# Kernel tuning notes

Hardware: AMD Instinct MI355X
Metric: run time of the kernel (lower is better)

Reference implementation:

```python
import jax, jax.numpy as jnp
import numpy as np

D = 1024
H = 16
HD = D // H  # 64


def gelu_custom(x):
    # Note: module uses 0.04715 (not the standard 0.044715) -- replicate exactly.
    c = jnp.sqrt(jnp.asarray(2.0 / jnp.pi, dtype=x.dtype))
    return 0.5 * x * (1.0 + jnp.tanh(c * (x + 0.04715 * x ** 3)))


def layernorm(x, scale, shift, eps=1e-5):
    u = jnp.mean(x, axis=-1, keepdims=True)
    v = jnp.var(x, axis=-1, keepdims=True)
    return scale * ((x - u) / jnp.sqrt(v + eps)) + shift


def setup_inputs() -> dict:
    key = jax.random.key(0)
    ks = jax.random.split(key, 12)
    s = 0.02
    X = jax.random.normal(ks[0], (4, 2048, D), dtype=jnp.float32)
    Wq = jax.random.normal(ks[1], (D, D), dtype=jnp.float32) * s
    Wk = jax.random.normal(ks[2], (D, D), dtype=jnp.float32) * s
    Wv = jax.random.normal(ks[3], (D, D), dtype=jnp.float32) * s
    Wo = jax.random.normal(ks[4], (D, D), dtype=jnp.float32) * s
    bo = jnp.zeros((D,), dtype=jnp.float32)
    W1 = jax.random.normal(ks[5], (D, 4 * D), dtype=jnp.float32) * s
    b1 = jnp.zeros((4 * D,), dtype=jnp.float32)
    W2 = jax.random.normal(ks[6], (4 * D, D), dtype=jnp.float32) * s
    b2 = jnp.zeros((D,), dtype=jnp.float32)
    g1 = jnp.ones((D,), dtype=jnp.float32)
    s1 = jnp.zeros((D,), dtype=jnp.float32)
    g2 = jnp.ones((D,), dtype=jnp.float32)
    s2 = jnp.zeros((D,), dtype=jnp.float32)
    return {"X": X, "Wq": Wq, "Wk": Wk, "Wv": Wv, "Wo": Wo, "bo": bo,
            "W1": W1, "b1": b1, "W2": W2, "b2": b2,
            "g1": g1, "s1": s1, "g2": g2, "s2": s2}


def reference(X, Wq, Wk, Wv, Wo, bo, W1, b1, W2, b2, g1, s1, g2, s2):
    b, n, _ = X.shape
    # --- pre-LN attention sublayer ---
    shortcut = X
    Y = layernorm(X, g1, s1)
    Q = (Y @ Wq).reshape(b, n, H, HD).transpose(0, 2, 1, 3)  # [b,h,n,hd]
    K = (Y @ Wk).reshape(b, n, H, HD).transpose(0, 2, 1, 3)
    V = (Y @ Wv).reshape(b, n, H, HD).transpose(0, 2, 1, 3)
    S = jnp.einsum('bhqd,bhkd->bhqk', Q, K)  # full eager score matrix
    causal = jnp.triu(jnp.ones((n, n), dtype=bool), k=1)
    S = jnp.where(causal, -jnp.inf, S)
    W = jax.nn.softmax(S / jnp.sqrt(jnp.asarray(HD, dtype=S.dtype)), axis=-1)
    Z = jnp.einsum('bhqk,bhkd->bhqd', W, V)
    Z = Z.transpose(0, 2, 1, 3).reshape(b, n, D)
    Z = Z @ Wo + bo
    X1 = Z + shortcut
    # --- pre-LN FFN sublayer ---
    Y2 = layernorm(X1, g2, s2)
    F = gelu_custom(Y2 @ W1 + b1) @ W2 + b2
    return F + X1
```

## Files before the change

### kernel.cpp

```cpp
#include <hip/hip_runtime.h>
#include <cstdint>
#include <cstddef>

#define DEV static __device__ __forceinline__

typedef __bf16 bf16x8 __attribute__((ext_vector_type(8)));
typedef float f32x4 __attribute__((ext_vector_type(4)));
typedef unsigned short u16x8 __attribute__((ext_vector_type(8)));
typedef unsigned short u16;

DEV u16 f2bf(float f) { __bf16 b = (__bf16)f; return __builtin_bit_cast(u16, b); }

DEV void async_cp16(const void* g, void* l) {
    __builtin_amdgcn_global_load_lds(
        (const __attribute__((address_space(1))) void*)g,
        (__attribute__((address_space(3))) void*)l, 16, 0, 0);
}

DEV void wait_vm6() { asm volatile("s_waitcnt vmcnt(6)" ::: "memory"); }
DEV void wait_vm4() { asm volatile("s_waitcnt vmcnt(4)" ::: "memory"); }
DEV void wait_vm0() { asm volatile("s_waitcnt vmcnt(0)" ::: "memory"); }

DEV float gelu_fn(float x) {
    const float c = 0.7978845608028654f;
    float t = c * (x + 0.04715f * x * x * x);
    float e = __expf(2.f * t);
    float th = 1.f - 2.f / (e + 1.f);
    return 0.5f * x * (1.f + th);
}

__global__ __launch_bounds__(256) void wtrans_all_kernel(
    const float* __restrict__ Wq, const float* __restrict__ Wk,
    const float* __restrict__ Wv, const float* __restrict__ Wo,
    const float* __restrict__ W1, const float* __restrict__ W2,
    u16* __restrict__ Wqkvt, u16* __restrict__ Wot,
    u16* __restrict__ W1t, u16* __restrict__ W2t)
{
    const int bid = blockIdx.x;
    const float* W;
    u16* Wt;
    int K, N, nx, loc;
    if (bid < 4096) {
        loc = bid & 1023;
        const int wsel = bid >> 10;
        W = (wsel == 0) ? Wq : (wsel == 1) ? Wk : (wsel == 2) ? Wv : Wo;
        Wt = (wsel == 3) ? Wot : (Wqkvt + (size_t)wsel * 1024 * 1024);
        K = 1024; N = 1024; nx = 32;
    } else if (bid < 8192) {
        loc = bid - 4096; W = W1; Wt = W1t; K = 1024; N = 4096; nx = 128;
    } else {
        loc = bid - 8192; W = W2; Wt = W2t; K = 4096; N = 1024; nx = 32;
    }
    const int n0 = (loc % nx) * 32, k0 = (loc / nx) * 32;

    __shared__ float t[32][33];
    const int tx = threadIdx.x & 31, ty = threadIdx.x >> 5;
#pragma unroll
    for (int i = 0; i < 4; ++i)
        t[ty + i * 8][tx] = W[(size_t)(k0 + ty + i * 8) * N + n0 + tx];
    __syncthreads();
#pragma unroll
    for (int i = 0; i < 4; ++i)
        Wt[(size_t)(n0 + ty + i * 8) * K + k0 + tx] = f2bf(t[tx][ty + i * 8]);
}

__global__ __launch_bounds__(256) void ln_kernel(
    const float* __restrict__ X, const float* __restrict__ g,
    const float* __restrict__ sh, u16* __restrict__ Y)
{
    int row = blockIdx.x;
    const float4* xr = (const float4*)(X + (size_t)row * 1024);
    float4 x = xr[threadIdx.x];
    float s = x.x + x.y + x.z + x.w;
    float ss = x.x * x.x + x.y * x.y + x.z * x.z + x.w * x.w;
#pragma unroll
    for (int off = 32; off >= 1; off >>= 1) {
        s += __shfl_xor(s, off);
        ss += __shfl_xor(ss, off);
    }
    __shared__ float ps[4], pss[4];
    int wave = threadIdx.x >> 6, lane = threadIdx.x & 63;
    if (lane == 0) { ps[wave] = s; pss[wave] = ss; }
    __syncthreads();
    s = ps[0] + ps[1] + ps[2] + ps[3];
    ss = pss[0] + pss[1] + pss[2] + pss[3];
    float mean = s * (1.f / 1024.f);
    float var = ss * (1.f / 1024.f) - mean * mean;
    float rstd = rsqrtf(var + 1e-5f);
    int c = threadIdx.x * 4;
    ushort4 o;
    o.x = f2bf((x.x - mean) * rstd * g[c + 0] + sh[c + 0]);
    o.y = f2bf((x.y - mean) * rstd * g[c + 1] + sh[c + 1]);
    o.z = f2bf((x.z - mean) * rstd * g[c + 2] + sh[c + 2]);
    o.w = f2bf((x.w - mean) * rstd * g[c + 3] + sh[c + 3]);
    ((ushort4*)(Y + (size_t)row * 1024))[threadIdx.x] = o;
}

template <int OUT_BF16, int HAS_BIAS, int HAS_RES, int ACT_GELU>
__global__ __launch_bounds__(256) void gemm_kernel(
    const u16* __restrict__ A, const u16* __restrict__ Bt,
    const float* __restrict__ bias, const float* __restrict__ res,
    void* __restrict__ Cout, int M, int N, int K)
{
    __shared__ u16 As[3][128 * 32];
    __shared__ u16 Bs[3][128 * 32];
    const int tid = threadIdx.x;
    const int lane = tid & 63, wave = tid >> 6;
    const int wm = wave >> 1, wn = wave & 1;
    const int l16 = lane & 15, lg = lane >> 4;
    const int rowBase = blockIdx.y * 128;
    const int colBase = blockIdx.x * 128;

    f32x4 acc[4][4];
#pragma unroll
    for (int m = 0; m < 4; ++m)
#pragma unroll
        for (int n = 0; n < 4; ++n) acc[m][n] = (f32x4){0.f, 0.f, 0.f, 0.f};

#define GSTAGE(SB, KT)                                                        \
    {                                                                         \
        _Pragma("unroll")                                                     \
        for (int i_ = 0; i_ < 2; ++i_) {                                      \
            int eo = tid * 8 + i_ * 2048;                                     \
            int r_ = eo >> 5, c_ = eo & 31;                                   \
            async_cp16(A + (size_t)(rowBase + r_) * K + (KT) + c_, As[SB] + eo); \
            async_cp16(Bt + (size_t)(colBase + r_) * K + (KT) + c_, Bs[SB] + eo); \
        }                                                                     \
    }

    const int nt = K >> 5;
    GSTAGE(0, 0);
    GSTAGE(1, 32);
    wait_vm4();
    __builtin_amdgcn_s_barrier();
    __builtin_amdgcn_sched_barrier(0);

    int cur = 0, stg = 2;
    for (int t = 0; t < nt; ++t) {
        const bool more = (t + 2 < nt);
        if (more) GSTAGE(stg, (t + 2) * 32);

        bf16x8 af[4], bfr[4];
#pragma unroll
        for (int m = 0; m < 4; ++m)
            af[m] = *(const bf16x8*)(As[cur] + (wm * 64 + m * 16 + l16) * 32 + lg * 8);
#pragma unroll
        for (int n = 0; n < 4; ++n)
            bfr[n] = *(const bf16x8*)(Bs[cur] + (wn * 64 + n * 16 + l16) * 32 + lg * 8);
#pragma unroll
        for (int m = 0; m < 4; ++m)
#pragma unroll
            for (int n = 0; n < 4; ++n)
                acc[m][n] = __builtin_amdgcn_mfma_f32_16x16x32_bf16(
                    af[m], bfr[n], acc[m][n], 0, 0, 0);

        if (more) wait_vm4(); else wait_vm0();
        __builtin_amdgcn_s_barrier();
        __builtin_amdgcn_sched_barrier(0);
        cur = (cur == 2) ? 0 : cur + 1;
        stg = (stg == 2) ? 0 : stg + 1;
    }
#undef GSTAGE

#pragma unroll
    for (int m = 0; m < 4; ++m) {
#pragma unroll
        for (int n = 0; n < 4; ++n) {
            int gr0 = rowBase + wm * 64 + m * 16 + lg * 4;
            int gc = colBase + wn * 64 + n * 16 + l16;
            float bv = HAS_BIAS ? bias[gc] : 0.f;
#pragma unroll
            for (int r = 0; r < 4; ++r) {
                float v = acc[m][n][r] + bv;
                if (ACT_GELU) v = gelu_fn(v);
                if (HAS_RES) v += res[(size_t)(gr0 + r) * N + gc];
                if (OUT_BF16)
                    ((u16*)Cout)[(size_t)(gr0 + r) * N + gc] = f2bf(v);
                else
                    ((float*)Cout)[(size_t)(gr0 + r) * N + gc] = v;
            }
        }
    }
}

template <int OUT_BF16, int HAS_BIAS, int ACT_GELU>
__global__ __launch_bounds__(512, 2) void gemm8p_kernel(
    const u16* __restrict__ A, const u16* __restrict__ Bt,
    const float* __restrict__ bias, void* __restrict__ Cout,
    int M, int N, int K)
{
    __shared__ u16 As[2][256 * 64];
    __shared__ u16 Bs[2][256 * 64];
    const int tid = threadIdx.x;
    const int lane = tid & 63, wave = tid >> 6;
    const int wm = wave >> 2, wn = wave & 3;
    const int l16 = lane & 15, lg = lane >> 4;

    const int gx = gridDim.x, gy = gridDim.y;
    const int nwg = gx * gy;
    const int orig = (int)blockIdx.y * gx + (int)blockIdx.x;
    const int work = (orig & 7) * (nwg >> 3) + (orig >> 3);
    const int colBase = (work / gy) * 256;
    const int rowBase = (work % gy) * 256;

    f32x4 acc[8][4];
#pragma unroll
    for (int m = 0; m < 8; ++m)
#pragma unroll
        for (int n = 0; n < 4; ++n) acc[m][n] = (f32x4){0.f, 0.f, 0.f, 0.f};

#define STRIP(SB, KT, S)                                                      \
    {                                                                         \
        int tl_ = tid & 255, hf_ = tid >> 8;                                  \
        int r_ = hf_ * 128 + (S) * 32 + (tl_ >> 3);                           \
        int gl_ = (tl_ & 7) ^ (r_ & 7);                                       \
        int dst_ = r_ * 64 + (tl_ & 7) * 8;                                   \
        async_cp16(A + (size_t)(rowBase + r_) * K + (KT) + gl_ * 8, As[SB] + dst_); \
        async_cp16(Bt + (size_t)(colBase + r_) * K + (KT) + gl_ * 8, Bs[SB] + dst_); \
    }
#define FRAG_OFF(row, G) ((row) * 64 + (((G) ^ ((row) & 7)) * 8))

#define PHASE(BUF, QUAD, LOADB, STAGE, WAITN)                                 \
    {                                                                         \
        __builtin_amdgcn_sched_barrier(0);                                    \
        if (LOADB) {                                                          \
            _Pragma("unroll")                                                 \
            for (int nf = 0; nf < 4; ++nf) {                                  \
                int row = wn * 64 + nf * 16 + l16;                            \
                _Pragma("unroll")                                             \
                for (int ks = 0; ks < 2; ++ks)                                \
                    bfr[nf][ks] = *(const bf16x8*)(Bs[BUF] + FRAG_OFF(row, lg + ks * 4)); \
            }                                                                 \
        }                                                                     \
        bf16x8 af[2][2];                                                      \
        _Pragma("unroll")                                                     \
        for (int mi = 0; mi < 2; ++mi) {                                      \
            int row = wm * 128 + (QUAD) * 32 + mi * 16 + l16;                 \
            _Pragma("unroll")                                                 \
            for (int ks = 0; ks < 2; ++ks)                                    \
                af[mi][ks] = *(const bf16x8*)(As[BUF] + FRAG_OFF(row, lg + ks * 4)); \
        }                                                                     \
        STAGE;                                                                \
        __builtin_amdgcn_sched_barrier(0);                                    \
        __builtin_amdgcn_s_barrier();                                         \
        __builtin_amdgcn_s_setprio(1);                                        \
        _Pragma("unroll")                                                     \
        for (int mi = 0; mi < 2; ++mi)                                        \
            _Pragma("unroll")                                                 \
            for (int nf = 0; nf < 4; ++nf)                                    \
                _Pragma("unroll")                                             \
                for (int ks = 0; ks < 2; ++ks)                                \
                    acc[(QUAD) * 2 + mi][nf] =                                \
                        __builtin_amdgcn_mfma_f32_16x16x32_bf16(              \
                            af[mi][ks], bfr[nf][ks], acc[(QUAD) * 2 + mi][nf], 0, 0, 0); \
        __builtin_amdgcn_s_setprio(0);                                        \
        __builtin_amdgcn_sched_barrier(0);                                    \
        WAITN;                                                                \
        __builtin_amdgcn_s_barrier();                                         \
    }

    const int nt = K >> 6;
    const int half = nt >> 1;

    STRIP(0, 0, 0); STRIP(0, 0, 1); STRIP(0, 0, 2); STRIP(0, 0, 3);
    STRIP(1, 64, 0); STRIP(1, 64, 1); STRIP(1, 64, 2);
    wait_vm6();
    __builtin_amdgcn_s_barrier();
    __builtin_amdgcn_sched_barrier(0);

    for (int it = 0; it < half; ++it) {
        const int kt1 = (it * 2 + 1) << 6;
        const int kt2 = (it * 2 + 2) << 6;
        const int kt3 = (it * 2 + 3) << 6;
        const bool more = (it + 1 < half);
        bf16x8 bfr[4][2];
        PHASE(0, 0, 1, STRIP(1, kt1, 3), ((void)0));
        PHASE(0, 1, 0, if (more) STRIP(0, kt2, 0), ((void)0));
        PHASE(0, 2, 0, if (more) STRIP(0, kt2, 1), ((void)0));
        PHASE(0, 3, 0, if (more) STRIP(0, kt2, 2),
              if (more) wait_vm6(); else wait_vm0());
        PHASE(1, 0, 1, if (more) STRIP(0, kt2, 3), ((void)0));
        PHASE(1, 1, 0, if (more) STRIP(1, kt3, 0), ((void)0));
        PHASE(1, 2, 0, if (more) STRIP(1, kt3, 1), ((void)0));
        PHASE(1, 3, 0, if (more) STRIP(1, kt3, 2),
              if (more) wait_vm6(); else wait_vm0());
    }
#undef STRIP
#undef FRAG_OFF
#undef PHASE

#pragma unroll
    for (int mf = 0; mf < 8; ++mf) {
#pragma unroll
        for (int nf = 0; nf < 4; ++nf) {
            int gr0 = rowBase + wm * 128 + mf * 16 + lg * 4;
            int gc = colBase + wn * 64 + nf * 16 + l16;
            float bv = HAS_BIAS ? bias[gc] : 0.f;
#pragma unroll
            for (int r = 0; r < 4; ++r) {
                float v = acc[mf][nf][r] + bv;
                if (ACT_GELU) v = gelu_fn(v);
                if (OUT_BF16)
                    ((u16*)Cout)[(size_t)(gr0 + r) * N + gc] = f2bf(v);
                else
                    ((float*)Cout)[(size_t)(gr0 + r) * N + gc] = v;
            }
        }
    }
}

__global__ __launch_bounds__(512) void attn_kernel(
    const u16* __restrict__ QKV, u16* __restrict__ Z)
{
    __shared__ u16 Ks[2][64 * 64];
    __shared__ u16 Vt[2][64 * 64];
    __shared__ u16 Pl[8][32 * 64];

    const int bh = blockIdx.x;
    const int b = bh >> 4, h = bh & 15;
    const int g = blockIdx.y;
    const int qt = (g < 4) ? (7 - g) : (g - 4);
    const int tid = threadIdx.x;
    const int wave = tid >> 6, lane = tid & 63;
    const int l16 = lane & 15, lg = lane >> 4;

    const size_t baseQ = (size_t)b * 2048 * 3072 + (size_t)h * 64;
    const size_t baseK = baseQ + 1024;
    const size_t baseV = baseQ + 2048;

    const int q0w = qt * 256 + wave * 32;

    bf16x8 aq[2][2];
#pragma unroll
    for (int mq = 0; mq < 2; ++mq) {
        const u16* qp = QKV + baseQ + (size_t)(q0w + mq * 16 + l16) * 3072;
#pragma unroll
        for (int hf = 0; hf < 2; ++hf) {
            bf16x8 v = *(const bf16x8*)(qp + hf * 32 + lg * 8);
#pragma unroll
            for (int j = 0; j < 8; ++j) v[j] = (__bf16)((float)v[j] * 0.125f);
            aq[mq][hf] = v;
        }
    }

    f32x4 o[2][4];
    float lrow[2][4];
#pragma unroll
    for (int mq = 0; mq < 2; ++mq)
#pragma unroll
        for (int i = 0; i < 4; ++i) {
            o[mq][i] = (f32x4){0.f, 0.f, 0.f, 0.f};
            lrow[mq][i] = 0.f;
        }

    const int nch = 4 * qt + 4;

#define STAGE_K(BUF, KB)                                                      \
    {                                                                         \
        int n = tid;                                                          \
        int r = n >> 3;                                                       \
        int lb = ((n & 7) * 16) ^ ((r & 7) << 4);                             \
        async_cp16(QKV + baseK + (size_t)((KB) + r) * 3072 + (lb >> 1),       \
                   Ks[BUF] + n * 8);                                          \
    }
#define LOAD_V(KB, V0)                                                        \
    {                                                                         \
        const u16* vp = QKV + baseV + (size_t)((KB) + lane) * 3072;           \
        V0 = *(const u16x8*)(vp + wave * 8);                                  \
    }
#define WRITE_V(BUF, V0)                                                      \
    {                                                                         \
        _Pragma("unroll")                                                     \
        for (int j = 0; j < 8; ++j) {                                         \
            int d = wave * 8 + j;                                             \
            int byt = (d * 128 + lane * 2) ^ ((d & 7) << 4);                  \
            Vt[BUF][byt >> 1] = V0[j];                                        \
        }                                                                     \
    }
#define SOFTMAX_BODY(DIAG)                                                    \
    _Pragma("unroll")                                                         \
    for (int mq = 0; mq < 2; ++mq) {                                          \
        _Pragma("unroll")                                                     \
        for (int r = 0; r < 4; ++r) {                                         \
            float sv0 = s[mq][0][r];                                          \
            float sv1 = s[mq][1][r];                                          \
            float sv2 = s[mq][2][r];                                          \
            float sv3 = s[mq][3][r];                                          \
            if (DIAG) {                                                       \
                const int q = q0w + mq * 16 + lg * 4 + r;                     \
                if (kbase + 0 + l16 > q)  sv0 = -1e30f;                       \
                if (kbase + 16 + l16 > q) sv1 = -1e30f;                       \
                if (kbase + 32 + l16 > q) sv2 = -1e30f;                       \
                if (kbase + 48 + l16 > q) sv3 = -1e30f;                       \
            }                                                                 \
            float p0 = __expf(sv0), p1 = __expf(sv1);                         \
            float p2 = __expf(sv2), p3 = __expf(sv3);                         \
            lrow[mq][r] += (p0 + p1) + (p2 + p3);                             \
            int rowm = mq * 16 + lg * 4 + r;                                  \
            int rb = rowm * 128, swz = (rowm & 7) << 4;                       \
            Pl[wave][(rb + ((0  + 2 * l16) ^ swz)) >> 1] = f2bf(p0);          \
            Pl[wave][(rb + ((32 + 2 * l16) ^ swz)) >> 1] = f2bf(p1);          \
            Pl[wave][(rb + ((64 + 2 * l16) ^ swz)) >> 1] = f2bf(p2);          \
            Pl[wave][(rb + ((96 + 2 * l16) ^ swz)) >> 1] = f2bf(p3);          \
        }                                                                     \
    }

    {
        STAGE_K(0, 0);
        u16x8 v0;
        LOAD_V(0, v0);
        WRITE_V(0, v0);
    }
    __syncthreads();

    int cur = 0;
    for (int kc = 0; kc < nch; ++kc) {
        const int kbase = kc * 64;
        const int nxt = cur ^ 1;
        const bool more = (kc + 1 < nch);
        u16x8 nv0;
        if (more) {
            STAGE_K(nxt, kbase + 64);
            LOAD_V(kbase + 64, nv0);
        }

        if (q0w + 31 >= kbase) {
            f32x4 s[2][4];
#pragma unroll
            for (int mq = 0; mq < 2; ++mq)
#pragma unroll
                for (int t = 0; t < 4; ++t) s[mq][t] = (f32x4){0.f, 0.f, 0.f, 0.f};
            __builtin_amdgcn_s_setprio(1);
#pragma unroll
            for (int t = 0; t < 4; ++t) {
                int row = t * 16 + l16;
                int swz = (row & 7) << 4;
                bf16x8 bk0 = *(const bf16x8*)(Ks[cur] + ((row * 128 + ((16 * lg) ^ swz)) >> 1));
                bf16x8 bk1 = *(const bf16x8*)(Ks[cur] + ((row * 128 + ((64 + 16 * lg) ^ swz)) >> 1));
#pragma unroll
                for (int mq = 0; mq < 2; ++mq) {
                    s[mq][t] = __builtin_amdgcn_mfma_f32_16x16x32_bf16(aq[mq][0], bk0, s[mq][t], 0, 0, 0);
                    s[mq][t] = __builtin_amdgcn_mfma_f32_16x16x32_bf16(aq[mq][1], bk1, s[mq][t], 0, 0, 0);
                }
            }
            __builtin_amdgcn_s_setprio(0);

            const bool diag = (kbase + 63 > q0w);
            if (diag) { SOFTMAX_BODY(1) } else { SOFTMAX_BODY(0) }

            bf16x8 bv[2][4];
#pragma unroll
            for (int kst = 0; kst < 2; ++kst)
#pragma unroll
                for (int ct = 0; ct < 4; ++ct) {
                    int d = ct * 16 + l16;
                    bv[kst][ct] = *(const bf16x8*)(Vt[cur] + ((d * 128 + ((64 * kst + 16 * lg) ^ ((d & 7) << 4))) >> 1));
                }
            __builtin_amdgcn_s_setprio(1);
#pragma unroll
            for (int mq = 0; mq < 2; ++mq) {
                int rowm = mq * 16 + l16;
                int swz = (rowm & 7) << 4;
                bf16x8 ap0 = *(const bf16x8*)(&Pl[wave][(rowm * 128 + ((16 * lg) ^ swz)) >> 1]);
                bf16x8 ap1 = *(const bf16x8*)(&Pl[wave][(rowm * 128 + ((64 + 16 * lg) ^ swz)) >> 1]);
#pragma unroll
                for (int ct = 0; ct < 4; ++ct) {
                    o[mq][ct] = __builtin_amdgcn_mfma_f32_16x16x32_bf16(ap0, bv[0][ct], o[mq][ct], 0, 0, 0);
                    o[mq][ct] = __builtin_amdgcn_mfma_f32_16x16x32_bf16(ap1, bv[1][ct], o[mq][ct], 0, 0, 0);
                }
            }
            __builtin_amdgcn_s_setprio(0);
        }

        if (more) { WRITE_V(nxt, nv0); }
        __syncthreads();
        cur = nxt;
    }

#pragma unroll
    for (int mq = 0; mq < 2; ++mq)
#pragma unroll
        for (int r = 0; r < 4; ++r) {
            float l = lrow[mq][r];
            l += __shfl_xor(l, 1);
            l += __shfl_xor(l, 2);
            l += __shfl_xor(l, 4);
            l += __shfl_xor(l, 8);
            float inv = 1.f / l;
            size_t zr = ((size_t)b * 2048 + q0w + mq * 16 + lg * 4 + r) * 1024 + h * 64;
#pragma unroll
            for (int ct = 0; ct < 4; ++ct)
                Z[zr + ct * 16 + l16] = f2bf(o[mq][ct][r] * inv);
        }
#undef STAGE_K
#undef LOAD_V
#undef WRITE_V
#undef SOFTMAX_BODY
}

extern "C" void kernel_launch(void* const* d_in, const int* in_sizes, int n_in,
                              void* d_out, int out_size, void* d_ws, size_t ws_size,
                              hipStream_t stream)
{
    const float* X  = (const float*)d_in[0];
    const float* Wq = (const float*)d_in[1];
    const float* Wk = (const float*)d_in[2];
    const float* Wv = (const float*)d_in[3];
    const float* Wo = (const float*)d_in[4];
    const float* bo = (const float*)d_in[5];
    const float* W1 = (const float*)d_in[6];
    const float* b1 = (const float*)d_in[7];
    const float* W2 = (const float*)d_in[8];
    const float* b2 = (const float*)d_in[9];
    const float* g1 = (const float*)d_in[10];
    const float* s1 = (const float*)d_in[11];
    const float* g2 = (const float*)d_in[12];
    const float* s2 = (const float*)d_in[13];
    float* out = (float*)d_out;

    uint8_t* ws = (uint8_t*)d_ws;
    const size_t MB = 1024 * 1024;
    u16* Wqkvt = (u16*)(ws + 0 * MB);
    u16* Wot   = (u16*)(ws + 6 * MB);
    u16* W1t   = (u16*)(ws + 8 * MB);
    u16* W2t   = (u16*)(ws + 16 * MB);
    u16* Yb    = (u16*)(ws + 24 * MB);
    u16* QKVb  = (u16*)(ws + 40 * MB);
    u16* Zb    = (u16*)(ws + 24 * MB);
    u16* Y2b   = (u16*)(ws + 40 * MB);
    u16* Hb    = (u16*)(ws + 56 * MB);

    wtrans_all_kernel<<<12288, 256, 0, stream>>>(Wq, Wk, Wv, Wo, W1, W2,
                                                 Wqkvt, Wot, W1t, W2t);

    ln_kernel<<<8192, 256, 0, stream>>>(X, g1, s1, Yb);

    gemm_kernel<1, 0, 0, 0><<<dim3(24, 64), 256, 0, stream>>>(Yb, Wqkvt, nullptr, nullptr, QKVb, 8192, 3072, 1024);

    attn_kernel<<<dim3(64, 8), 512, 0, stream>>>(QKVb, Zb);

    gemm_kernel<0, 1, 1, 0><<<dim3(8, 64), 256, 0, stream>>>(Zb, Wot, bo, X, out, 8192, 1024, 1024);

    ln_kernel<<<8192, 256, 0, stream>>>(out, g2, s2, Y2b);

    gemm8p_kernel<1, 1, 1><<<dim3(16, 32), 512, 0, stream>>>(Y2b, W1t, b1, Hb, 8192, 4096, 1024);

    gemm_kernel<0, 1, 1, 0><<<dim3(8, 64), 256, 0, stream>>>(Hb, W2t, b2, out, out, 8192, 1024, 4096);
}
```

Baseline: 408.4 us.

## Run FFN down-projection with split-K on the 256x256 GEMM plus combine kernel

The W2 GEMM (K=4096) moves from the 128x128 gemm_kernel to the larger 256x256 gemm8p kernel with a 2-way split-K. Each half writes a bf16 partial into the workspace, and a new combine kernel adds both partials, the bias and the residual into the output. The goal is to use the more efficient large-tile kernel while still launching enough workgroups (256) to fill the device. In exchange it adds an extra kernel launch and extra memory traffic for the partials. Storing the partials in bf16 also loses some precision before accumulation.

New measurement: 381.1 us. -6.7%, faster.

```diff
diff --git a/kernel.cpp b/kernel.cpp
--- a/kernel.cpp
+++ b/kernel.cpp
@@ -10,6 +10,7 @@
 typedef unsigned short u16;
 
 DEV u16 f2bf(float f) { __bf16 b = (__bf16)f; return __builtin_bit_cast(u16, b); }
+DEV float bf2f(u16 u) { unsigned v = (unsigned)u << 16; return __builtin_bit_cast(float, v); }
 
 DEV void async_cp16(const void* g, void* l) {
     __builtin_amdgcn_global_load_lds(
@@ -96,6 +97,23 @@
     ((ushort4*)(Y + (size_t)row * 1024))[threadIdx.x] = o;
 }
 
+__global__ __launch_bounds__(256) void combine_kernel(
+    const u16* __restrict__ P0, const u16* __restrict__ P1,
+    const float* __restrict__ b2, float* __restrict__ out)
+{
+    const size_t row = blockIdx.x;
+    const int c = threadIdx.x * 4;
+    const size_t off = row * 1024 + c;
+    ushort4 a = *(const ushort4*)(P0 + off);
+    ushort4 b = *(const ushort4*)(P1 + off);
+    float4 o = *(float4*)(out + off);
+    o.x += bf2f(a.x) + bf2f(b.x) + b2[c + 0];
+    o.y += bf2f(a.y) + bf2f(b.y) + b2[c + 1];
+    o.z += bf2f(a.z) + bf2f(b.z) + b2[c + 2];
+    o.w += bf2f(a.w) + bf2f(b.w) + b2[c + 3];
+    *(float4*)(out + off) = o;
+}
+
 template <int OUT_BF16, int HAS_BIAS, int HAS_RES, int ACT_GELU>
 __global__ __launch_bounds__(256) void gemm_kernel(
     const u16* __restrict__ A, const u16* __restrict__ Bt,
@@ -187,7 +205,7 @@
 __global__ __launch_bounds__(512, 2) void gemm8p_kernel(
     const u16* __restrict__ A, const u16* __restrict__ Bt,
     const float* __restrict__ bias, void* __restrict__ Cout,
-    int M, int N, int K)
+    int M, int N, int K, int ldk, int rowTiles, int koff, size_t coff)
 {
     __shared__ u16 As[2][256 * 64];
     __shared__ u16 Bs[2][256 * 64];
@@ -201,7 +219,11 @@
     const int orig = (int)blockIdx.y * gx + (int)blockIdx.x;
     const int work = (orig & 7) * (nwg >> 3) + (orig >> 3);
     const int colBase = (work / gy) * 256;
-    const int rowBase = (work % gy) * 256;
+    const int wy = work % gy;
+    const int rowBase = (wy % rowTiles) * 256;
+    const int ks = wy / rowTiles;
+    A += (size_t)ks * koff;
+    Bt += (size_t)ks * koff;
 
     f32x4 acc[8][4];
 #pragma unroll
@@ -215,8 +237,8 @@
         int r_ = hf_ * 128 + (S) * 32 + (tl_ >> 3);                           \
         int gl_ = (tl_ & 7) ^ (r_ & 7);                                       \
         int dst_ = r_ * 64 + (tl_ & 7) * 8;                                   \
-        async_cp16(A + (size_t)(rowBase + r_) * K + (KT) + gl_ * 8, As[SB] + dst_); \
-        async_cp16(Bt + (size_t)(colBase + r_) * K + (KT) + gl_ * 8, Bs[SB] + dst_); \
+        async_cp16(A + (size_t)(rowBase + r_) * ldk + (KT) + gl_ * 8, As[SB] + dst_); \
+        async_cp16(Bt + (size_t)(colBase + r_) * ldk + (KT) + gl_ * 8, Bs[SB] + dst_); \
     }
 #define FRAG_OFF(row, G) ((row) * 64 + (((G) ^ ((row) & 7)) * 8))
 
@@ -228,8 +250,8 @@
             for (int nf = 0; nf < 4; ++nf) {                                  \
                 int row = wn * 64 + nf * 16 + l16;                            \
                 _Pragma("unroll")                                             \
-                for (int ks = 0; ks < 2; ++ks)                                \
-                    bfr[nf][ks] = *(const bf16x8*)(Bs[BUF] + FRAG_OFF(row, lg + ks * 4)); \
+                for (int ks_ = 0; ks_ < 2; ++ks_)                             \
+                    bfr[nf][ks_] = *(const bf16x8*)(Bs[BUF] + FRAG_OFF(row, lg + ks_ * 4)); \
             }                                                                 \
         }                                                                     \
         bf16x8 af[2][2];                                                      \
@@ -237,8 +259,8 @@
         for (int mi = 0; mi < 2; ++mi) {                                      \
             int row = wm * 128 + (QUAD) * 32 + mi * 16 + l16;                 \
             _Pragma("unroll")                                                 \
-            for (int ks = 0; ks < 2; ++ks)                                    \
-                af[mi][ks] = *(const bf16x8*)(As[BUF] + FRAG_OFF(row, lg + ks * 4)); \
+            for (int ks_ = 0; ks_ < 2; ++ks_)                                 \
+                af[mi][ks_] = *(const bf16x8*)(As[BUF] + FRAG_OFF(row, lg + ks_ * 4)); \
         }                                                                     \
         STAGE;                                                                \
         __builtin_amdgcn_sched_barrier(0);                                    \
@@ -249,10 +271,10 @@
             _Pragma("unroll")                                                 \
             for (int nf = 0; nf < 4; ++nf)                                    \
                 _Pragma("unroll")                                             \
-                for (int ks = 0; ks < 2; ++ks)                                \
+                for (int ks_ = 0; ks_ < 2; ++ks_)                             \
                     acc[(QUAD) * 2 + mi][nf] =                                \
                         __builtin_amdgcn_mfma_f32_16x16x32_bf16(              \
-                            af[mi][ks], bfr[nf][ks], acc[(QUAD) * 2 + mi][nf], 0, 0, 0); \
+                            af[mi][ks_], bfr[nf][ks_], acc[(QUAD) * 2 + mi][nf], 0, 0, 0); \
         __builtin_amdgcn_s_setprio(0);                                        \
         __builtin_amdgcn_sched_barrier(0);                                    \
         WAITN;                                                                \
@@ -301,9 +323,9 @@
                 float v = acc[mf][nf][r] + bv;
                 if (ACT_GELU) v = gelu_fn(v);
                 if (OUT_BF16)
-                    ((u16*)Cout)[(size_t)(gr0 + r) * N + gc] = f2bf(v);
+                    ((u16*)Cout)[(size_t)ks * coff + (size_t)(gr0 + r) * N + gc] = f2bf(v);
                 else
-                    ((float*)Cout)[(size_t)(gr0 + r) * N + gc] = v;
+                    ((float*)Cout)[(size_t)ks * coff + (size_t)(gr0 + r) * N + gc] = v;
             }
         }
     }
@@ -529,6 +551,7 @@
     u16* Zb    = (u16*)(ws + 24 * MB);
     u16* Y2b   = (u16*)(ws + 40 * MB);
     u16* Hb    = (u16*)(ws + 56 * MB);
+    u16* Pk    = (u16*)(ws + 24 * MB);
 
     wtrans_all_kernel<<<12288, 256, 0, stream>>>(Wq, Wk, Wv, Wo, W1, W2,
                                                  Wqkvt, Wot, W1t, W2t);
@@ -543,7 +566,11 @@
 
     ln_kernel<<<8192, 256, 0, stream>>>(out, g2, s2, Y2b);
 
-    gemm8p_kernel<1, 1, 1><<<dim3(16, 32), 512, 0, stream>>>(Y2b, W1t, b1, Hb, 8192, 4096, 1024);
-
-    gemm_kernel<0, 1, 1, 0><<<dim3(8, 64), 256, 0, stream>>>(Hb, W2t, b2, out, out, 8192, 1024, 4096);
-}
+    gemm8p_kernel<1, 1, 1><<<dim3(16, 32), 512, 0, stream>>>(
+        Y2b, W1t, b1, Hb, 8192, 4096, 1024, 1024, 32, 0, 0);
+
+    gemm8p_kernel<1, 0, 0><<<dim3(4, 64), 512, 0, stream>>>(
+        Hb, W2t, nullptr, Pk, 8192, 1024, 2048, 4096, 32, 2048, (size_t)8192 * 1024);
+
+    combine_kernel<<<8192, 256, 0, stream>>>(Pk, Pk + (size_t)8192 * 1024, b2, out);
+}
```
